# Kernel tuning notes

Measured on AMD Instinct MI355X. Metric: run time of the kernel, lower is better.

The kernel has to match this reference:

```python
import jax, jax.numpy as jnp
import numpy as np
import math

B, T, D, H = 4, 2048, 1024, 16
ND = D // H  # head dim = 64


def setup_inputs() -> dict:
    key = jax.random.key(0)
    ks = jax.random.split(key, 12)
    s = 1.0 / math.sqrt(D)
    inp = {
        "q": jax.random.normal(ks[0], (B, T, D), jnp.float32),
        "k": jax.random.normal(ks[1], (B, T, D), jnp.float32),
        "v": jax.random.normal(ks[2], (B, T, D), jnp.float32),
        # nn.Linear params: weight [out,in], bias [out]
        "wq": jax.random.normal(ks[3], (D, D), jnp.float32) * s,
        "bq": jax.random.normal(ks[4], (D,), jnp.float32) * s,
        "wk": jax.random.normal(ks[5], (D, D), jnp.float32) * s,
        "bk": jax.random.normal(ks[6], (D,), jnp.float32) * s,
        "wv": jax.random.normal(ks[7], (D, D), jnp.float32) * s,
        "bv": jax.random.normal(ks[8], (D,), jnp.float32) * s,
        "wo": jax.random.normal(ks[9], (D, D), jnp.float32) * s,
        "bo": jax.random.normal(ks[10], (D,), jnp.float32) * s,
        # causal mask: 1 where attending allowed, 0 -> -inf
        "mask": jnp.tril(jnp.ones((T, T), jnp.int32)),
    }
    return inp


def reference(q, k, v, wq, bq, wk, bk, wv, bv, wo, bo, mask):
    batch, time, dim = q.shape
    n_d = dim // H
    # NOTE: original module (faithfully reproduced bug) computes k and v from q
    Q = q @ wq.T + bq
    K = q @ wk.T + bk
    V = q @ wv.T + bv
    # [B, T, D] -> [B, H, T, nd]
    Q = Q.reshape(batch, time, H, n_d).transpose(0, 2, 1, 3)
    K = K.reshape(batch, time, H, n_d).transpose(0, 2, 1, 3)
    V = V.reshape(batch, time, H, n_d).transpose(0, 2, 1, 3)
    score = jnp.einsum("bhqd,bhkd->bhqk", Q, K) / math.sqrt(n_d)
    score = jnp.where(mask == 0, -jnp.inf, score)
    # original uses nn.Softmax(dim=-2): normalize over the QUERY axis
    attn = jax.nn.softmax(score, axis=-2)
    out = jnp.einsum("bhqk,bhkd->bhqd", attn, V)
    out = out.transpose(0, 2, 1, 3).reshape(batch, time, dim)
    return out @ wo.T + bo
```

## Files before the change

kernel.cpp:

```cpp
#include <hip/hip_runtime.h>
#include <stdint.h>

#define B_  4
#define T_  2048
#define D_  1024
#define H_  16
#define ND_ 64
#define M_  (B_ * T_)

typedef unsigned short u16;
typedef __bf16 bf8  __attribute__((ext_vector_type(8)));
typedef float  f4   __attribute__((ext_vector_type(4)));
typedef u16    u16x8 __attribute__((ext_vector_type(8)));

__device__ inline float bf2f(u16 b) {
    unsigned int x = ((unsigned int)b) << 16;
    return __builtin_bit_cast(float, x);
}
__device__ inline u16 f2bf(float f) {
    unsigned int x = __builtin_bit_cast(unsigned int, f);
    x += 0x7fffu + ((x >> 16) & 1u);
    return (u16)(x >> 16);
}
__device__ inline f4 mfma16(bf8 a, bf8 b, f4 c) {
    return __builtin_amdgcn_mfma_f32_16x16x32_bf16(a, b, c, 0, 0, 0);
}
__device__ inline void async16(const void* g, void* l) {
    auto gp = reinterpret_cast<const __attribute__((address_space(1))) unsigned int*>(
        reinterpret_cast<uintptr_t>(g));
    auto lp = reinterpret_cast<__attribute__((address_space(3))) unsigned int*>(
        reinterpret_cast<uintptr_t>(l));
    __builtin_amdgcn_global_load_lds(gp, lp, 16, 0, 0);
}

__global__ __launch_bounds__(256)
void cvt_bf16(const float* __restrict__ in, u16* __restrict__ out, int n) {
    int i = (blockIdx.x * blockDim.x + threadIdx.x) * 8;
    if (i + 8 <= n) {
        float4 a = *(const float4*)(in + i);
        float4 b = *(const float4*)(in + i + 4);
        u16x8 o;
        o[0] = f2bf(a.x); o[1] = f2bf(a.y); o[2] = f2bf(a.z); o[3] = f2bf(a.w);
        o[4] = f2bf(b.x); o[5] = f2bf(b.y); o[6] = f2bf(b.z); o[7] = f2bf(b.w);
        *(u16x8*)(out + i) = o;
    }
}

template <int MODE>
__global__ __launch_bounds__(256, 2)
void gemm_bt(const u16* __restrict__ A, const u16* __restrict__ W,
             const float* __restrict__ bias, void* __restrict__ CoutV) {
    constexpr int K = 1024;
    constexpr int N = 1024;
    __shared__ __attribute__((aligned(16))) u16 sA[128 * 32];
    __shared__ __attribute__((aligned(16))) u16 sB[128 * 32];
    const int tid  = threadIdx.x;
    const int wave = tid >> 6;
    const int lane = tid & 63;
    const int m0 = blockIdx.y * 128;
    const int n0 = blockIdx.x * 128;
    const int wm = (wave & 1) * 64;
    const int wn = (wave >> 1) * 64;

    f4 acc[4][4] = {};

    const int srow = wave * 32 + (lane >> 2);
    const int scol = (lane & 3) * 8;
    const u16* gA = A + (size_t)(m0 + srow) * K + scol;
    const u16* gB = W + (size_t)(n0 + srow) * K + scol;
    u16* lA0 = sA + (wave * 32) * 32;
    u16* lA1 = sA + (wave * 32 + 16) * 32;
    u16* lB0 = sB + (wave * 32) * 32;
    u16* lB1 = sB + (wave * 32 + 16) * 32;

    const int row = lane & 15;
    const int qo  = (lane >> 4) * 8;

    for (int k0 = 0; k0 < K; k0 += 32) {
        async16(gA + k0, lA0);
        async16(gA + k0 + (size_t)16 * K, lA1);
        async16(gB + k0, lB0);
        async16(gB + k0 + (size_t)16 * K, lB1);
        __syncthreads();

        bf8 af[4], bfr[4];
#pragma unroll
        for (int i = 0; i < 4; i++)
            af[i] = *(const bf8*)(sA + (wm + i * 16 + row) * 32 + qo);
#pragma unroll
        for (int i = 0; i < 4; i++)
            bfr[i] = *(const bf8*)(sB + (wn + i * 16 + row) * 32 + qo);
#pragma unroll
        for (int mi = 0; mi < 4; mi++)
#pragma unroll
            for (int ni = 0; ni < 4; ni++)
                acc[mi][ni] = mfma16(af[mi], bfr[ni], acc[mi][ni]);
        __syncthreads();
    }

#pragma unroll
    for (int ni = 0; ni < 4; ni++) {
        const int n = n0 + wn + ni * 16 + row;
        const float bv = bias[n];
#pragma unroll
        for (int mi = 0; mi < 4; mi++) {
#pragma unroll
            for (int r = 0; r < 4; r++) {
                const int m = m0 + wm + mi * 16 + (lane >> 4) * 4 + r;
                const float v = acc[mi][ni][r] + bv;
                if (MODE == 1) {
                    size_t idx = (((size_t)((m >> 11) * H_ + (n >> 6)) * T_) + (m & (T_ - 1))) * ND_ +
                                 (n & (ND_ - 1));
                    ((u16*)CoutV)[idx] = f2bf(v);
                } else if (MODE == 2) {
                    size_t idx = ((size_t)(((m >> 11) * H_ + (n >> 6)) * ND_ + (n & (ND_ - 1)))) * T_ +
                                 (m & (T_ - 1));
                    ((u16*)CoutV)[idx] = f2bf(v);
                } else {
                    ((float*)CoutV)[(size_t)m * N + n] = v;
                }
            }
        }
    }
}

__global__ __launch_bounds__(256)
void col_sum(const u16* __restrict__ Qh, const u16* __restrict__ Kh,
             float* __restrict__ Ic) {
    __shared__ __attribute__((aligned(16))) u16 sQ[2][32 * 72];
    const int bh   = blockIdx.y;
    const int tid  = threadIdx.x;
    const int wave = tid >> 6;
    const int lane = tid & 63;
    const int l15  = lane & 15;
    const int quad = lane >> 4;
    const int qo   = quad * 8;
    const int sr   = tid >> 3;
    const int sc   = (tid & 7) * 8;
    const u16* Qb = Qh + (size_t)bh * T_ * ND_;
    const u16* Kb = Kh + (size_t)bh * T_ * ND_;

#pragma unroll
    for (int half = 0; half < 2; half++) {
        const int strip = half ? (15 - (int)blockIdx.x) : (int)blockIdx.x;
        const int c0  = strip * 128;
        const int c0w = c0 + wave * 32;
        bf8 b0[2], b1[2];
#pragma unroll
        for (int g = 0; g < 2; g++) {
            b0[g] = *(const bf8*)(Kb + (size_t)(c0w + g * 16 + l15) * ND_ + qo);
            b1[g] = *(const bf8*)(Kb + (size_t)(c0w + g * 16 + l15) * ND_ + 32 + qo);
        }
        float acc[2][4] = {};
        int p = 0;
        u16x8 pq = *(const u16x8*)(Qb + (size_t)(c0 + sr) * ND_ + sc);
        for (int qt = c0; qt < T_; qt += 32) {
            *(u16x8*)(&sQ[p][sr * 72 + sc]) = pq;
            __syncthreads();
            if (qt + 32 < T_)
                pq = *(const u16x8*)(Qb + (size_t)(qt + 32 + sr) * ND_ + sc);
            const bool masked = qt < c0 + 128;
#pragma unroll
            for (int sub = 0; sub < 2; sub++) {
                const int rho = sub * 16 + l15;
                bf8 a0 = *(const bf8*)(&sQ[p][rho * 72 + qo]);
                bf8 a1 = *(const bf8*)(&sQ[p][rho * 72 + 32 + qo]);
#pragma unroll
                for (int g = 0; g < 2; g++) {
                    f4 s = {0.f, 0.f, 0.f, 0.f};
                    s = mfma16(a0, b0[g], s);
                    s = mfma16(a1, b1[g], s);
                    if (masked) {
#pragma unroll
                        for (int r = 0; r < 4; r++) {
                            const int qg = qt + sub * 16 + quad * 4 + r;
                            const int cg = c0w + g * 16 + l15;
                            acc[g][r] += (qg >= cg) ? __expf(s[r] * 0.125f) : 0.f;
                        }
                    } else {
#pragma unroll
                        for (int r = 0; r < 4; r++)
                            acc[g][r] += __expf(s[r] * 0.125f);
                    }
                }
            }
            p ^= 1;
        }
        __syncthreads();
#pragma unroll
        for (int g = 0; g < 2; g++) {
            float l = acc[g][0] + acc[g][1] + acc[g][2] + acc[g][3];
            l += __shfl_xor(l, 16);
            l += __shfl_xor(l, 32);
            if (lane < 16) Ic[(size_t)bh * T_ + c0w + g * 16 + l15] = 1.f / l;
        }
    }
}

__global__ __launch_bounds__(256, 4)
void attn_out(const u16* __restrict__ Qh, const u16* __restrict__ Kh,
              const u16* __restrict__ Vt, const float* __restrict__ Ic,
              u16* __restrict__ AO) {
    __shared__ __attribute__((aligned(16))) u16 sK[64 * 72];
    __shared__ __attribute__((aligned(16))) u16 sVt[64 * 72];
    __shared__ __attribute__((aligned(16))) u16 sP[4][32 * 72];
    const int bh   = blockIdx.x;
    const int b    = bh >> 4;
    const int h    = bh & 15;
    const int qb   = (int)(gridDim.y - 1 - blockIdx.y) * 128;
    const int tid  = threadIdx.x;
    const int wave = tid >> 6;
    const int lane = tid & 63;
    const int l15  = lane & 15;
    const int quad = lane >> 4;
    const int qo   = quad * 8;

    const u16* Qb = Qh + (size_t)bh * T_ * ND_;
    const u16* Kb = Kh + (size_t)bh * T_ * ND_;
    const u16* Vb = Vt + (size_t)bh * ND_ * T_;
    const float* ic = Ic + (size_t)bh * T_;

    const int qw = qb + wave * 32;
    bf8 aq[2][2];
#pragma unroll
    for (int qs = 0; qs < 2; qs++)
#pragma unroll
        for (int dh = 0; dh < 2; dh++)
            aq[qs][dh] = *(const bf8*)(Qb + (size_t)(qw + qs * 16 + l15) * ND_ + dh * 32 + qo);

    f4 o[2][4] = {};

    const int sr = tid >> 3;
    const int sc = (tid & 7) * 8;
    const int kend = qb + 128;

    u16x8 pk0 = *(const u16x8*)(Kb + (size_t)sr * ND_ + sc);
    u16x8 pk1 = *(const u16x8*)(Kb + (size_t)(sr + 32) * ND_ + sc);
    u16x8 pv0 = *(const u16x8*)(Vb + (size_t)sr * T_ + sc);
    u16x8 pv1 = *(const u16x8*)(Vb + (size_t)(sr + 32) * T_ + sc);

    for (int kt = 0; kt < kend; kt += 64) {
        *(u16x8*)(sK + sr * 72 + sc) = pk0;
        *(u16x8*)(sK + (sr + 32) * 72 + sc) = pk1;
        *(u16x8*)(sVt + sr * 72 + sc) = pv0;
        *(u16x8*)(sVt + (sr + 32) * 72 + sc) = pv1;
        __syncthreads();

        const int ktn = kt + 64;
        if (ktn < kend) {
            pk0 = *(const u16x8*)(Kb + (size_t)(ktn + sr) * ND_ + sc);
            pk1 = *(const u16x8*)(Kb + (size_t)(ktn + sr + 32) * ND_ + sc);
            pv0 = *(const u16x8*)(Vb + (size_t)sr * T_ + ktn + sc);
            pv1 = *(const u16x8*)(Vb + (size_t)(sr + 32) * T_ + ktn + sc);
        }

#pragma unroll
        for (int ks = 0; ks < 4; ks++) {
            bf8 kb0 = *(const bf8*)(sK + (ks * 16 + l15) * 72 + qo);
            bf8 kb1 = *(const bf8*)(sK + (ks * 16 + l15) * 72 + 32 + qo);
            const int kg = kt + ks * 16 + l15;
            const float il = ic[kg];
#pragma unroll
            for (int qs = 0; qs < 2; qs++) {
                f4 s = {0.f, 0.f, 0.f, 0.f};
                s = mfma16(aq[qs][0], kb0, s);
                s = mfma16(aq[qs][1], kb1, s);
#pragma unroll
                for (int r = 0; r < 4; r++) {
                    const int qg = qw + qs * 16 + quad * 4 + r;
                    const float p = (kg <= qg) ? __expf(s[r] * 0.125f) * il : 0.f;
                    sP[wave][(qs * 16 + quad * 4 + r) * 72 + ks * 16 + l15] = f2bf(p);
                }
            }
        }
#pragma unroll
        for (int st = 0; st < 2; st++) {
            bf8 ap0 = *(const bf8*)(&sP[wave][(l15) * 72 + st * 32 + qo]);
            bf8 ap1 = *(const bf8*)(&sP[wave][(16 + l15) * 72 + st * 32 + qo]);
#pragma unroll
            for (int ds = 0; ds < 4; ds++) {
                bf8 bv = *(const bf8*)(sVt + (ds * 16 + l15) * 72 + st * 32 + qo);
                o[0][ds] = mfma16(ap0, bv, o[0][ds]);
                o[1][ds] = mfma16(ap1, bv, o[1][ds]);
            }
        }
        __syncthreads();
    }

#pragma unroll
    for (int qs = 0; qs < 2; qs++)
#pragma unroll
        for (int ds = 0; ds < 4; ds++)
#pragma unroll
            for (int r = 0; r < 4; r++) {
                const int q = qw + qs * 16 + quad * 4 + r;
                const int d = ds * 16 + l15;
                AO[((size_t)(b * T_ + q)) * D_ + h * ND_ + d] = f2bf(o[qs][ds][r]);
            }
}

extern "C" void kernel_launch(void* const* d_in, const int* in_sizes, int n_in,
                              void* d_out, int out_size, void* d_ws, size_t ws_size,
                              hipStream_t stream) {
    (void)in_sizes; (void)n_in; (void)out_size; (void)ws_size;
    const float* q  = (const float*)d_in[0];
    const float* wq = (const float*)d_in[3];
    const float* bq = (const float*)d_in[4];
    const float* wk = (const float*)d_in[5];
    const float* bk = (const float*)d_in[6];
    const float* wv = (const float*)d_in[7];
    const float* bv = (const float*)d_in[8];
    const float* wo = (const float*)d_in[9];
    const float* bo = (const float*)d_in[10];

    const size_t SZ = (size_t)M_ * D_;
    const size_t WSZ = (size_t)D_ * D_;
    u16* Qh  = (u16*)d_ws;
    u16* Kh  = Qh + SZ;
    u16* Vtr = Kh + SZ;
    u16* qbf = Vtr + SZ;
    u16* AO  = qbf;
    u16* wqb = qbf + SZ;
    u16* wkb = wqb + WSZ;
    u16* wvb = wkb + WSZ;
    u16* wob = wvb + WSZ;
    float* Ic = (float*)(wob + WSZ);

    cvt_bf16<<<dim3(SZ / 8 / 256), 256, 0, stream>>>(q, qbf, (int)SZ);
    cvt_bf16<<<dim3(WSZ / 8 / 256), 256, 0, stream>>>(wq, wqb, (int)WSZ);
    cvt_bf16<<<dim3(WSZ / 8 / 256), 256, 0, stream>>>(wk, wkb, (int)WSZ);
    cvt_bf16<<<dim3(WSZ / 8 / 256), 256, 0, stream>>>(wv, wvb, (int)WSZ);
    cvt_bf16<<<dim3(WSZ / 8 / 256), 256, 0, stream>>>(wo, wob, (int)WSZ);

    dim3 gp(D_ / 128, M_ / 128);
    gemm_bt<1><<<gp, 256, 0, stream>>>(qbf, wqb, bq, Qh);
    gemm_bt<1><<<gp, 256, 0, stream>>>(qbf, wkb, bk, Kh);
    gemm_bt<2><<<gp, 256, 0, stream>>>(qbf, wvb, bv, Vtr);

    dim3 gcs(8, B_ * H_);
    col_sum<<<gcs, 256, 0, stream>>>(Qh, Kh, Ic);

    dim3 ga(B_ * H_, T_ / 128);
    attn_out<<<ga, 256, 0, stream>>>(Qh, Kh, Vtr, Ic, AO);

    gemm_bt<0><<<gp, 256, 0, stream>>>(AO, wob, bo, d_out);
}
```

Measured before the change: 399.6 us.

## Fold softmax scale into Q projection, transpose score MFMA, merge weight conversions

Merges the four weight fp32-to-bf16 conversion launches into one kernel with a y-dimension selector. Folds the 1/sqrt(d) scale into the Q projection epilogue, so the column-sum and attention kernels no longer multiply scores. In attn_out the score MFMA operands are swapped so each lane holds four consecutive keys. This allows a vector load of the inverse column sums, a mask-free path for fully unmasked tiles, and packed bf16 conversion with 8-byte LDS stores instead of scalar stores. Scaling Q before bf16 rounding is exact for a power-of-two factor, but the packed conversion instruction may round differently from the software f2bf.

```diff
diff --git a/kernel.cpp b/kernel.cpp
--- a/kernel.cpp
+++ b/kernel.cpp
@@ -21,6 +21,11 @@
     unsigned int x = __builtin_bit_cast(unsigned int, f);
     x += 0x7fffu + ((x >> 16) & 1u);
     return (u16)(x >> 16);
+}
+__device__ inline unsigned int cvt_pk_bf16(float a, float b) {
+    unsigned int r;
+    asm("v_cvt_pk_bf16_f32 %0, %1, %2" : "=v"(r) : "v"(a), "v"(b));
+    return r;
 }
 __device__ inline f4 mfma16(bf8 a, bf8 b, f4 c) {
     return __builtin_amdgcn_mfma_f32_16x16x32_bf16(a, b, c, 0, 0, 0);
@@ -44,6 +49,27 @@
         o[4] = f2bf(b.x); o[5] = f2bf(b.y); o[6] = f2bf(b.z); o[7] = f2bf(b.w);
         *(u16x8*)(out + i) = o;
     }
+}
+
+__global__ __launch_bounds__(256)
+void cvt_w4(const float* __restrict__ w0, const float* __restrict__ w1,
+            const float* __restrict__ w2, const float* __restrict__ w3,
+            u16* __restrict__ o0, u16* __restrict__ o1,
+            u16* __restrict__ o2, u16* __restrict__ o3) {
+    const float* in; u16* out;
+    switch (blockIdx.y) {
+        case 0:  in = w0; out = o0; break;
+        case 1:  in = w1; out = o1; break;
+        case 2:  in = w2; out = o2; break;
+        default: in = w3; out = o3; break;
+    }
+    int i = (blockIdx.x * blockDim.x + threadIdx.x) * 8;
+    float4 a = *(const float4*)(in + i);
+    float4 b = *(const float4*)(in + i + 4);
+    u16x8 o;
+    o[0] = f2bf(a.x); o[1] = f2bf(a.y); o[2] = f2bf(a.z); o[3] = f2bf(a.w);
+    o[4] = f2bf(b.x); o[5] = f2bf(b.y); o[6] = f2bf(b.z); o[7] = f2bf(b.w);
+    *(u16x8*)(out + i) = o;
 }
 
 template <int MODE>
@@ -107,8 +133,9 @@
 #pragma unroll
             for (int r = 0; r < 4; r++) {
                 const int m = m0 + wm + mi * 16 + (lane >> 4) * 4 + r;
-                const float v = acc[mi][ni][r] + bv;
-                if (MODE == 1) {
+                float v = acc[mi][ni][r] + bv;
+                if (MODE == 3) v *= 0.125f;
+                if (MODE == 1 || MODE == 3) {
                     size_t idx = (((size_t)((m >> 11) * H_ + (n >> 6)) * T_) + (m & (T_ - 1))) * ND_ +
                                  (n & (ND_ - 1));
                     ((u16*)CoutV)[idx] = f2bf(v);
@@ -175,12 +202,12 @@
                         for (int r = 0; r < 4; r++) {
                             const int qg = qt + sub * 16 + quad * 4 + r;
                             const int cg = c0w + g * 16 + l15;
-                            acc[g][r] += (qg >= cg) ? __expf(s[r] * 0.125f) : 0.f;
+                            acc[g][r] += (qg >= cg) ? __expf(s[r]) : 0.f;
                         }
                     } else {
 #pragma unroll
                         for (int r = 0; r < 4; r++)
-                            acc[g][r] += __expf(s[r] * 0.125f);
+                            acc[g][r] += __expf(s[r]);
                     }
                 }
             }
@@ -258,19 +285,27 @@
         for (int ks = 0; ks < 4; ks++) {
             bf8 kb0 = *(const bf8*)(sK + (ks * 16 + l15) * 72 + qo);
             bf8 kb1 = *(const bf8*)(sK + (ks * 16 + l15) * 72 + 32 + qo);
-            const int kg = kt + ks * 16 + l15;
-            const float il = ic[kg];
+            const f4 icv = *(const f4*)(ic + kt + ks * 16 + quad * 4);
+            const int kbase = kt + ks * 16 + quad * 4;
 #pragma unroll
             for (int qs = 0; qs < 2; qs++) {
                 f4 s = {0.f, 0.f, 0.f, 0.f};
-                s = mfma16(aq[qs][0], kb0, s);
-                s = mfma16(aq[qs][1], kb1, s);
-#pragma unroll
-                for (int r = 0; r < 4; r++) {
-                    const int qg = qw + qs * 16 + quad * 4 + r;
-                    const float p = (kg <= qg) ? __expf(s[r] * 0.125f) * il : 0.f;
-                    sP[wave][(qs * 16 + quad * 4 + r) * 72 + ks * 16 + l15] = f2bf(p);
+                s = mfma16(kb0, aq[qs][0], s);
+                s = mfma16(kb1, aq[qs][1], s);
+                f4 p;
+                if (kt + ks * 16 + 15 <= qw + qs * 16) {
+#pragma unroll
+                    for (int r = 0; r < 4; r++) p[r] = __expf(s[r]) * icv[r];
+                } else {
+                    const int qg = qw + qs * 16 + l15;
+#pragma unroll
+                    for (int r = 0; r < 4; r++)
+                        p[r] = (kbase + r <= qg) ? __expf(s[r]) * icv[r] : 0.f;
                 }
+                uint2 w;
+                w.x = cvt_pk_bf16(p[0], p[1]);
+                w.y = cvt_pk_bf16(p[2], p[3]);
+                *(uint2*)(sP[wave] + (qs * 16 + l15) * 72 + ks * 16 + quad * 4) = w;
             }
         }
 #pragma unroll
@@ -327,13 +362,11 @@
     float* Ic = (float*)(wob + WSZ);
 
     cvt_bf16<<<dim3(SZ / 8 / 256), 256, 0, stream>>>(q, qbf, (int)SZ);
-    cvt_bf16<<<dim3(WSZ / 8 / 256), 256, 0, stream>>>(wq, wqb, (int)WSZ);
-    cvt_bf16<<<dim3(WSZ / 8 / 256), 256, 0, stream>>>(wk, wkb, (int)WSZ);
-    cvt_bf16<<<dim3(WSZ / 8 / 256), 256, 0, stream>>>(wv, wvb, (int)WSZ);
-    cvt_bf16<<<dim3(WSZ / 8 / 256), 256, 0, stream>>>(wo, wob, (int)WSZ);
+    cvt_w4<<<dim3(WSZ / 8 / 256, 4), 256, 0, stream>>>(wq, wk, wv, wo,
+                                                       wqb, wkb, wvb, wob);
 
     dim3 gp(D_ / 128, M_ / 128);
-    gemm_bt<1><<<gp, 256, 0, stream>>>(qbf, wqb, bq, Qh);
+    gemm_bt<3><<<gp, 256, 0, stream>>>(qbf, wqb, bq, Qh);
     gemm_bt<1><<<gp, 256, 0, stream>>>(qbf, wkb, bk, Kh);
     gemm_bt<2><<<gp, 256, 0, stream>>>(qbf, wvb, bv, Vtr);
 
```

Result: faster. 388.9 us (-2.7%).
